# Performance work log

Hardware: AMD Instinct MI355X
Metric: run time of the kernel (lower is better)

Reference implementation:

```python
import jax, jax.numpy as jnp
import numpy as np

NUM_HEADS = 12
TOPK = 90


def setup_inputs() -> dict:
    key = jax.random.key(0)
    k1, k2, k3 = jax.random.split(key, 3)
    B, N, C = 8, 512, 768
    x = jax.random.normal(k1, (B, N, C), dtype=jnp.float32)
    qkv_w = jax.random.normal(k2, (3 * C, C), dtype=jnp.float32) * (C ** -0.5)
    proj_w = jax.random.normal(k3, (C, C), dtype=jnp.float32) * (C ** -0.5)
    proj_b = jnp.zeros((C,), dtype=jnp.float32)
    return {"x": x, "qkv_w": qkv_w, "proj_w": proj_w, "proj_b": proj_b, "islast": 0}


def reference(x, qkv_w, proj_w, proj_b, islast):
    B, N, C = x.shape
    H = NUM_HEADS
    hd = C // H
    scale = hd ** -0.5
    # qkv projection (no bias), split into q,k,v heads: [B,H,N,hd]
    qkv = (x @ qkv_w.T).reshape(B, N, 3, H, hd).transpose(2, 0, 3, 1, 4)
    q, k, v = qkv[0], qkv[1], qkv[2]
    attn = jnp.einsum('bhnd,bhmd->bhnm', q, k) * scale  # [B,H,N,N]
    if not islast:
        # keep only the top-k scores per row (kth-value threshold == topk mask)
        kth = jax.lax.top_k(attn, TOPK)[0][..., -1:]  # [B,H,N,1]
        attn = jnp.where(attn >= kth, attn, -jnp.inf)
    attn = jax.nn.softmax(attn, axis=-1)
    out = jnp.einsum('bhnm,bhmd->bnhd', attn, v).reshape(B, N, C)
    out = out @ proj_w.T + proj_b
    return out, attn
```

## Files before the change

### kernel.cpp

```cpp
#include <hip/hip_runtime.h>
#include <math.h>

#define BB 8
#define NN 512
#define CC 768
#define HH 12
#define HD 64
#define TOPK 90
#define QKV_ELEMS (BB*HH*NN*HD)
#define KC 2304

typedef __attribute__((ext_vector_type(8))) short short8;
typedef __attribute__((ext_vector_type(4))) float floatx4;

__device__ inline unsigned short f2bf(float f) {
    unsigned int u = __float_as_uint(f);
    u += 0x7FFFu + ((u >> 16) & 1u);
    return (unsigned short)(u >> 16);
}
__device__ inline float bf2f(unsigned short h) {
    return __uint_as_float(((unsigned int)h) << 16);
}

template<bool IS_A>
__global__ __launch_bounds__(256) void split_k(const float* __restrict__ in,
                                               unsigned short* __restrict__ o2,
                                               int total) {
    int idx = blockIdx.x * 256 + threadIdx.x;
    if (idx >= total) return;
    int e = idx * 4;
    int m = e / CC, kk = e - m * CC;
    float4 f = *(const float4*)(in + e);
    ushort4 hi, lo;
    hi.x = f2bf(f.x); lo.x = f2bf(f.x - bf2f(hi.x));
    hi.y = f2bf(f.y); lo.y = f2bf(f.y - bf2f(hi.y));
    hi.z = f2bf(f.z); lo.z = f2bf(f.z - bf2f(hi.z));
    hi.w = f2bf(f.w); lo.w = f2bf(f.w - bf2f(hi.w));
    unsigned short* base = o2 + (size_t)m * KC + kk;
    *(ushort4*)(base)        = hi;
    *(ushort4*)(base + CC)   = IS_A ? hi : lo;
    *(ushort4*)(base + 2*CC) = IS_A ? lo : hi;
}

template<int NCOLS, bool QKV_EPI>
__global__ __launch_bounds__(256) void gemm_split(const unsigned short* __restrict__ A,
                                                  const unsigned short* __restrict__ Bm,
                                                  const float* __restrict__ bias,
                                                  float* __restrict__ out,
                                                  unsigned short* __restrict__ qh,
                                                  unsigned short* __restrict__ ql,
                                                  unsigned short* __restrict__ kh,
                                                  unsigned short* __restrict__ kl,
                                                  float* __restrict__ vt) {
    __shared__ char lds[16384];
    const int bm = blockIdx.x, bn = blockIdx.y;
    const int tid  = threadIdx.x;
    const int wave = tid >> 6, lane = tid & 63;
    const int wm = wave >> 1, wn = wave & 1;
    const int quad = lane >> 4, r = lane & 15;

    const int cA0 = tid, cA1 = tid + 256;
    const int mA0 = cA0 >> 2, oA0 = (cA0 & 3) ^ ((mA0 >> 1) & 3);
    const int mA1 = cA1 >> 2, oA1 = (cA1 & 3) ^ ((mA1 >> 1) & 3);
    const unsigned short* gA0 = A  + (size_t)(bm*128 + mA0) * KC + oA0*8;
    const unsigned short* gA1 = A  + (size_t)(bm*128 + mA1) * KC + oA1*8;
    const unsigned short* gB0 = Bm + (size_t)(bn*128 + mA0) * KC + oA0*8;
    const unsigned short* gB1 = Bm + (size_t)(bn*128 + mA1) * KC + oA1*8;
    char* lA0 = lds + (wave*64)*16;
    char* lA1 = lds + (256 + wave*64)*16;
    char* lB0 = lds + 8192 + (wave*64)*16;
    char* lB1 = lds + 8192 + (256 + wave*64)*16;

    const int octsel = quad ^ ((r >> 1) & 3);
    int aoff[4], boff[4];
#pragma unroll
    for (int i = 0; i < 4; ++i) {
        aoff[i] = ((wm*64 + i*16 + r)*4 + octsel) * 16;
        boff[i] = 8192 + ((wn*64 + i*16 + r)*4 + octsel) * 16;
    }

    floatx4 acc[4][4];
#pragma unroll
    for (int i = 0; i < 4; ++i)
#pragma unroll
        for (int j = 0; j < 4; ++j)
            acc[i][j] = (floatx4){0.f, 0.f, 0.f, 0.f};

    for (int it = 0; it < KC/32; ++it) {
        __syncthreads();
        __builtin_amdgcn_global_load_lds((const __attribute__((address_space(1))) unsigned int*)gA0,
                                         (__attribute__((address_space(3))) unsigned int*)lA0, 16, 0, 0);
        __builtin_amdgcn_global_load_lds((const __attribute__((address_space(1))) unsigned int*)gA1,
                                         (__attribute__((address_space(3))) unsigned int*)lA1, 16, 0, 0);
        __builtin_amdgcn_global_load_lds((const __attribute__((address_space(1))) unsigned int*)gB0,
                                         (__attribute__((address_space(3))) unsigned int*)lB0, 16, 0, 0);
        __builtin_amdgcn_global_load_lds((const __attribute__((address_space(1))) unsigned int*)gB1,
                                         (__attribute__((address_space(3))) unsigned int*)lB1, 16, 0, 0);
        gA0 += 32; gA1 += 32; gB0 += 32; gB1 += 32;
        asm volatile("s_waitcnt vmcnt(0)" ::: "memory");
        __syncthreads();

        short8 af[4], bf[4];
#pragma unroll
        for (int i = 0; i < 4; ++i) af[i] = *(const short8*)(lds + aoff[i]);
#pragma unroll
        for (int j = 0; j < 4; ++j) bf[j] = *(const short8*)(lds + boff[j]);
#pragma unroll
        for (int i = 0; i < 4; ++i)
#pragma unroll
            for (int j = 0; j < 4; ++j)
                acc[i][j] = __builtin_amdgcn_mfma_f32_16x16x32_bf16(af[i], bf[j], acc[i][j], 0, 0, 0);
    }

    if (QKV_EPI) {
#pragma unroll
        for (int j = 0; j < 4; ++j) {
            int col = bn*128 + wn*64 + j*16 + r;
            int t = col / CC;
            int rem = col - t*CC;
            int h = rem >> 6, d = rem & 63;
            if (t == 2) {
#pragma unroll
                for (int i = 0; i < 4; ++i) {
                    int m0 = bm*128 + wm*64 + i*16 + quad*4;
                    int b = m0 >> 9, n0 = m0 & 511;
                    float4 o4 = {acc[i][j][0], acc[i][j][1], acc[i][j][2], acc[i][j][3]};
                    *(float4*)(vt + ((size_t)((b*HH + h)*HD + d))*NN + n0) = o4;
                }
            } else {
                unsigned short* ph = (t == 0) ? qh : kh;
                unsigned short* pl = (t == 0) ? ql : kl;
#pragma unroll
                for (int i = 0; i < 4; ++i) {
#pragma unroll
                    for (int e = 0; e < 4; ++e) {
                        int m = bm*128 + wm*64 + i*16 + quad*4 + e;
                        int b = m >> 9, nrow = m & 511;
                        size_t idx = ((size_t)(b*HH + h)*NN + nrow)*HD + d;
                        float val = acc[i][j][e];
                        unsigned short hi = f2bf(val);
                        ph[idx] = hi;
                        pl[idx] = f2bf(val - bf2f(hi));
                    }
                }
            }
        }
    } else {
#pragma unroll
        for (int j = 0; j < 4; ++j) {
            int col = bn*128 + wn*64 + j*16 + r;
            float bv = bias[col];
#pragma unroll
            for (int i = 0; i < 4; ++i) {
#pragma unroll
                for (int e = 0; e < 4; ++e) {
                    int m = bm*128 + wm*64 + i*16 + quad*4 + e;
                    out[(size_t)m*NCOLS + col] = acc[i][j][e] + bv;
                }
            }
        }
    }
}

__global__ __launch_bounds__(256, 1) void attn_scores_k(
        const unsigned short* __restrict__ qh, const unsigned short* __restrict__ ql,
        const unsigned short* __restrict__ kh, const unsigned short* __restrict__ kl,
        const int* __restrict__ islast, float* __restrict__ attn) {

    __shared__ unsigned short qs[2][64][72];
    __shared__ char ks[16384];

    const int bh = blockIdx.x % 96;
    const int rb = blockIdx.x / 96;
    const int tid = threadIdx.x;
    const int wv = tid >> 6, lane = tid & 63;
    const int quad = lane >> 4, r = lane & 15;

    const unsigned short* gq[2] = { qh + ((size_t)bh*NN + rb*64)*HD,
                                    ql + ((size_t)bh*NN + rb*64)*HD };
#pragma unroll
    for (int i = 0; i < 4; ++i) {
        int s = tid + i*256;
        int hl = s >> 9, s2 = s & 511;
        int row = s2 >> 3, oct = s2 & 7;
        short8 val = *(const short8*)(gq[hl] + row*HD + oct*8);
        *(short8*)&qs[hl][row][oct*8] = val;
    }
    __syncthreads();

    short8 afr[6];
    {
        const int arow = wv*16 + r;
#pragma unroll
        for (int t = 0; t < 3; ++t) {
            int src = (t == 2) ? 1 : 0;
#pragma unroll
            for (int half = 0; half < 2; ++half)
                afr[t*2+half] = *(const short8*)&qs[src][arow][half*32 + quad*8];
        }
    }

    floatx4 acc[32];
#pragma unroll
    for (int ct = 0; ct < 32; ++ct) acc[ct] = (floatx4){0.f,0.f,0.f,0.f};

    const unsigned short* gk[2] = { kh + (size_t)bh*NN*HD, kl + (size_t)bh*NN*HD };

    for (int ch = 0; ch < 8; ++ch) {
        __syncthreads();
#pragma unroll
        for (int i = 0; i < 4; ++i) {
            int s = tid + i*256;
            int hl = s >> 9, s2 = s & 511;
            int row = s2 >> 3, octp = s2 & 7;
            int oct = octp ^ (row & 7);
            const unsigned short* src = gk[hl] + (size_t)(ch*64 + row)*HD + oct*8;
            __builtin_amdgcn_global_load_lds(
                (const __attribute__((address_space(1))) unsigned int*)src,
                (__attribute__((address_space(3))) unsigned int*)(ks + (size_t)(i*256 + wv*64)*16),
                16, 0, 0);
        }
        asm volatile("s_waitcnt vmcnt(0)" ::: "memory");
        __syncthreads();

#pragma unroll
        for (int ctl = 0; ctl < 4; ++ctl) {
            const int ct = ch*4 + ctl;
            const int n = ctl*16 + r;
#pragma unroll
            for (int t = 0; t < 3; ++t) {
                const int srcB = (t == 1) ? 1 : 0;
#pragma unroll
                for (int half = 0; half < 2; ++half) {
                    const int oct = (half*4 + quad) ^ (n & 7);
                    short8 bfr = *(const short8*)(ks + srcB*8192 + n*128 + oct*16);
                    acc[ct] = __builtin_amdgcn_mfma_f32_16x16x32_bf16(afr[t*2+half], bfr, acc[ct], 0, 0, 0);
                }
            }
        }
    }

    const int lastv = islast[0];

#pragma unroll
    for (int e = 0; e < 4; ++e) {
        unsigned int key[32];
#pragma unroll
        for (int ct = 0; ct < 32; ++ct) {
            unsigned int t = __float_as_uint(acc[ct][e] * 0.125f);
            key[ct] = (t & 0x80000000u) ? ~t : (t | 0x80000000u);
        }

        unsigned int kth = 0u;
        if (!lastv) {
            unsigned int uo = key[0], ua = key[0];
#pragma unroll
            for (int ct = 1; ct < 32; ++ct) { uo |= key[ct]; ua &= key[ct]; }
#pragma unroll
            for (int off = 1; off <= 8; off <<= 1) {
                uo |= __shfl_xor(uo, off);
                ua &= __shfl_xor(ua, off);
            }
            unsigned int diff = uo ^ ua;
            int bit = 31 - __clz(diff);
            unsigned int am = 0xFFFFFFFFu;
            int kk = TOPK, cntA = 512;
            int done = (diff == 0u);
            while (__ballot(!done) != 0ull) {
                if (!done) {
                    unsigned int m1 = 0u;
#pragma unroll
                    for (int ct = 0; ct < 32; ++ct)
                        m1 |= ((key[ct] >> bit) & 1u) << ct;
                    int c1 = __popc(am & m1);
                    c1 += __shfl_xor(c1, 1);
                    c1 += __shfl_xor(c1, 2);
                    c1 += __shfl_xor(c1, 4);
                    c1 += __shfl_xor(c1, 8);
                    if (kk <= c1) { am &= m1; cntA = c1; }
                    else          { kk -= c1; am &= ~m1; cntA -= c1; }
                    --bit;
                    done = (cntA == kk) | (kk == 1) | (bit < 0);
                }
            }
            unsigned int mn = 0xFFFFFFFFu, mx = 0u;
#pragma unroll
            for (int ct = 0; ct < 32; ++ct) {
                if ((am >> ct) & 1u) {
                    mn = mn < key[ct] ? mn : key[ct];
                    mx = mx > key[ct] ? mx : key[ct];
                }
            }
#pragma unroll
            for (int off = 1; off <= 8; off <<= 1) {
                unsigned int mns = __shfl_xor(mn, off), mxs = __shfl_xor(mx, off);
                mn = mn < mns ? mn : mns; mx = mx > mxs ? mx : mxs;
            }
            kth = (kk == 1) ? mx : mn;
        }

        unsigned int umx = key[0];
#pragma unroll
        for (int ct = 1; ct < 32; ++ct) umx = umx > key[ct] ? umx : key[ct];
#pragma unroll
        for (int off = 1; off <= 8; off <<= 1) {
            unsigned int t2 = __shfl_xor(umx, off);
            umx = umx > t2 ? umx : t2;
        }
        float fmx = __uint_as_float((umx & 0x80000000u) ? (umx & 0x7FFFFFFFu) : ~umx);
        float sum = 0.f;
#pragma unroll
        for (int ct = 0; ct < 32; ++ct) {
            unsigned int uu = key[ct];
            float f = __uint_as_float((uu & 0x80000000u) ? (uu & 0x7FFFFFFFu) : ~uu);
            float ev = (lastv || uu >= kth) ? __expf(f - fmx) : 0.f;
            acc[ct][e] = ev;
            sum += ev;
        }
#pragma unroll
        for (int off = 1; off <= 8; off <<= 1) sum += __shfl_xor(sum, off);
        const float inv = 1.f / sum;
        float* arow = attn + ((size_t)bh*NN + rb*64 + wv*16 + quad*4 + e) * NN;
#pragma unroll
        for (int ct = 0; ct < 32; ++ct) arow[ct*16 + r] = acc[ct][e] * inv;
    }
}

__global__ __launch_bounds__(256) void attn_pv_k(const float* __restrict__ attn,
                                                 const float* __restrict__ vt,
                                                 unsigned short* __restrict__ Ao) {
    __shared__ unsigned short pls[64][72];
    __shared__ unsigned short vhs[64][72];
    __shared__ unsigned short vls[64][72];

    const int blk = blockIdx.x;
    const int bh  = blk % 96;
    const int rb  = blk / 96;
    const int b = bh / HH, h = bh % HH;
    const int tid = threadIdx.x;
    const int wv = tid >> 6, lane = tid & 63;
    const int quad = lane >> 4, r = lane & 15;

    const int sm = tid >> 2;
    const int sk = (tid & 3) * 16;
    const float* prow = attn + ((size_t)bh*NN + rb*64 + sm) * NN + sk;
    const float* vrow = vt + ((size_t)bh*HD + sm) * NN + sk;

    floatx4 accO[4];
#pragma unroll
    for (int j = 0; j < 4; ++j) accO[j] = (floatx4){0.f,0.f,0.f,0.f};

    for (int ch = 0; ch < 8; ++ch) {
        float pv[16], vv[16];
#pragma unroll
        for (int x = 0; x < 4; ++x) {
            *(float4*)&pv[x*4] = *(const float4*)(prow + ch*64 + x*4);
            *(float4*)&vv[x*4] = *(const float4*)(vrow + ch*64 + x*4);
        }
        __syncthreads();
        unsigned short tp[16], th[16], tl[16];
#pragma unroll
        for (int x = 0; x < 16; ++x) {
            tp[x] = f2bf(pv[x]);
            th[x] = f2bf(vv[x]);
            tl[x] = f2bf(vv[x] - bf2f(th[x]));
        }
        *(short8*)&pls[sm][sk]   = *(short8*)&tp[0];
        *(short8*)&pls[sm][sk+8] = *(short8*)&tp[8];
        *(short8*)&vhs[sm][sk]   = *(short8*)&th[0];
        *(short8*)&vhs[sm][sk+8] = *(short8*)&th[8];
        *(short8*)&vls[sm][sk]   = *(short8*)&tl[0];
        *(short8*)&vls[sm][sk+8] = *(short8*)&tl[8];
        __syncthreads();

#pragma unroll
        for (int kb = 0; kb < 2; ++kb) {
            short8 af = *(const short8*)&pls[wv*16 + r][kb*32 + quad*8];
#pragma unroll
            for (int j = 0; j < 4; ++j) {
                short8 bh8 = *(const short8*)&vhs[j*16 + r][kb*32 + quad*8];
                short8 bl8 = *(const short8*)&vls[j*16 + r][kb*32 + quad*8];
                accO[j] = __builtin_amdgcn_mfma_f32_16x16x32_bf16(af, bh8, accO[j], 0, 0, 0);
                accO[j] = __builtin_amdgcn_mfma_f32_16x16x32_bf16(af, bl8, accO[j], 0, 0, 0);
            }
        }
    }

#pragma unroll
    for (int j = 0; j < 4; ++j) {
        int d = j*16 + r;
#pragma unroll
        for (int e = 0; e < 4; ++e) {
            int n = rb*64 + wv*16 + quad*4 + e;
            size_t mrow = (size_t)b*NN + n;
            float val = accO[j][e];
            unsigned short hi = f2bf(val);
            unsigned short lo = f2bf(val - bf2f(hi));
            unsigned short* base = Ao + mrow*KC + h*HD + d;
            base[0] = hi; base[CC] = hi; base[2*CC] = lo;
        }
    }
}

extern "C" void kernel_launch(void* const* d_in, const int* in_sizes, int n_in,
                              void* d_out, int out_size, void* d_ws, size_t ws_size,
                              hipStream_t stream) {
    const float* x      = (const float*)d_in[0];
    const float* qkv_w  = (const float*)d_in[1];
    const float* proj_w = (const float*)d_in[2];
    const float* proj_b = (const float*)d_in[3];
    const int*   islast = (const int*)d_in[4];

    float* out  = (float*)d_out;
    float* attn = out + (size_t)BB*NN*CC;

    float* ws = (float*)d_ws;
    float* vt = ws;
    unsigned short* qhp = (unsigned short*)(ws + (size_t)QKV_ELEMS);
    unsigned short* qlp = qhp + (size_t)QKV_ELEMS;
    unsigned short* khp = qlp + (size_t)QKV_ELEMS;
    unsigned short* klp = khp + (size_t)QKV_ELEMS;
    unsigned short* Asp   = klp + (size_t)QKV_ELEMS;
    unsigned short* Bqkv  = Asp  + (size_t)4096*KC;
    unsigned short* Bproj = Bqkv + (size_t)2304*KC;

    split_k<true> <<<dim3(4096*CC/4/256), 256, 0, stream>>>(x,      Asp,   4096*CC/4);
    split_k<false><<<dim3(2304*CC/4/256), 256, 0, stream>>>(qkv_w,  Bqkv,  2304*CC/4);
    split_k<false><<<dim3(CC*CC/4/256),   256, 0, stream>>>(proj_w, Bproj, CC*CC/4);

    gemm_split<0, true>  <<<dim3(32, 18), 256, 0, stream>>>(Asp, Bqkv, nullptr, nullptr,
                                                            qhp, qlp, khp, klp, vt);
    attn_scores_k        <<<dim3(96*8),   256, 0, stream>>>(qhp, qlp, khp, klp, islast, attn);
    attn_pv_k            <<<dim3(96*8),   256, 0, stream>>>(attn, vt, Asp);
    gemm_split<CC, false><<<dim3(32, 6),  256, 0, stream>>>(Asp, Bproj, proj_b, out,
                                                            nullptr, nullptr, nullptr, nullptr, nullptr);
}
```

Baseline: 366.2 us.

## Fuse PV into scores kernel, pre-split V to bf16, deepen GEMM K-tile

Merges the attention-probability times V step into the scores kernel so the normalized probabilities stay in registers instead of being re-read from global memory. The QKV GEMM epilogue now writes V transposed as bf16 hi/lo pairs, so the fused kernel can stream V tiles straight into LDS with global_load_lds. The GEMM K-step grows from 32 to 64, using 32KB of LDS with an 8-way XOR swizzle, which halves the number of barrier and wait round-trips. The costs are higher LDS and register pressure in the fused kernel and one fewer launch-level stage of parallelism.

Result: faster. 356.3 us (-2.7%).

```diff
diff --git a/kernel.cpp b/kernel.cpp
--- a/kernel.cpp
+++ b/kernel.cpp
@@ -51,33 +51,35 @@
                                                   unsigned short* __restrict__ ql,
                                                   unsigned short* __restrict__ kh,
                                                   unsigned short* __restrict__ kl,
-                                                  float* __restrict__ vt) {
-    __shared__ char lds[16384];
+                                                  unsigned short* __restrict__ vth,
+                                                  unsigned short* __restrict__ vtl) {
+    __shared__ char lds[32768];
     const int bm = blockIdx.x, bn = blockIdx.y;
     const int tid  = threadIdx.x;
     const int wave = tid >> 6, lane = tid & 63;
     const int wm = wave >> 1, wn = wave & 1;
     const int quad = lane >> 4, r = lane & 15;
 
-    const int cA0 = tid, cA1 = tid + 256;
-    const int mA0 = cA0 >> 2, oA0 = (cA0 & 3) ^ ((mA0 >> 1) & 3);
-    const int mA1 = cA1 >> 2, oA1 = (cA1 & 3) ^ ((mA1 >> 1) & 3);
-    const unsigned short* gA0 = A  + (size_t)(bm*128 + mA0) * KC + oA0*8;
-    const unsigned short* gA1 = A  + (size_t)(bm*128 + mA1) * KC + oA1*8;
-    const unsigned short* gB0 = Bm + (size_t)(bn*128 + mA0) * KC + oA0*8;
-    const unsigned short* gB1 = Bm + (size_t)(bn*128 + mA1) * KC + oA1*8;
-    char* lA0 = lds + (wave*64)*16;
-    char* lA1 = lds + (256 + wave*64)*16;
-    char* lB0 = lds + 8192 + (wave*64)*16;
-    char* lB1 = lds + 8192 + (256 + wave*64)*16;
-
-    const int octsel = quad ^ ((r >> 1) & 3);
-    int aoff[4], boff[4];
-#pragma unroll
-    for (int i = 0; i < 4; ++i) {
-        aoff[i] = ((wm*64 + i*16 + r)*4 + octsel) * 16;
-        boff[i] = 8192 + ((wn*64 + i*16 + r)*4 + octsel) * 16;
-    }
+    const unsigned short* gbase[8];
+#pragma unroll
+    for (int i = 0; i < 8; ++i) {
+        int c = tid + i*256;
+        int s = c & 1023;
+        int m = s >> 3, octp = s & 7, oct = octp ^ (m & 7);
+        gbase[i] = (i < 4 ? A  + (size_t)(bm*128 + m) * KC
+                          : Bm + (size_t)(bn*128 + m) * KC) + oct*8;
+    }
+
+    int aoff[2][4], boff[2][4];
+#pragma unroll
+    for (int kb = 0; kb < 2; ++kb)
+#pragma unroll
+        for (int i = 0; i < 4; ++i) {
+            int ra = wm*64 + i*16 + r;
+            int rb2 = wn*64 + i*16 + r;
+            aoff[kb][i] = (ra*8 + ((kb*4 + quad) ^ (ra & 7))) * 16;
+            boff[kb][i] = 16384 + (rb2*8 + ((kb*4 + quad) ^ (rb2 & 7))) * 16;
+        }
 
     floatx4 acc[4][4];
 #pragma unroll
@@ -86,30 +88,32 @@
         for (int j = 0; j < 4; ++j)
             acc[i][j] = (floatx4){0.f, 0.f, 0.f, 0.f};
 
-    for (int it = 0; it < KC/32; ++it) {
-        __syncthreads();
-        __builtin_amdgcn_global_load_lds((const __attribute__((address_space(1))) unsigned int*)gA0,
-                                         (__attribute__((address_space(3))) unsigned int*)lA0, 16, 0, 0);
-        __builtin_amdgcn_global_load_lds((const __attribute__((address_space(1))) unsigned int*)gA1,
-                                         (__attribute__((address_space(3))) unsigned int*)lA1, 16, 0, 0);
-        __builtin_amdgcn_global_load_lds((const __attribute__((address_space(1))) unsigned int*)gB0,
-                                         (__attribute__((address_space(3))) unsigned int*)lB0, 16, 0, 0);
-        __builtin_amdgcn_global_load_lds((const __attribute__((address_space(1))) unsigned int*)gB1,
-                                         (__attribute__((address_space(3))) unsigned int*)lB1, 16, 0, 0);
-        gA0 += 32; gA1 += 32; gB0 += 32; gB1 += 32;
+    for (int it = 0; it < KC/64; ++it) {
+        __syncthreads();
+#pragma unroll
+        for (int i = 0; i < 8; ++i) {
+            __builtin_amdgcn_global_load_lds(
+                (const __attribute__((address_space(1))) unsigned int*)gbase[i],
+                (__attribute__((address_space(3))) unsigned int*)(lds + i*4096 + wave*1024),
+                16, 0, 0);
+            gbase[i] += 64;
+        }
         asm volatile("s_waitcnt vmcnt(0)" ::: "memory");
         __syncthreads();
 
-        short8 af[4], bf[4];
-#pragma unroll
-        for (int i = 0; i < 4; ++i) af[i] = *(const short8*)(lds + aoff[i]);
-#pragma unroll
-        for (int j = 0; j < 4; ++j) bf[j] = *(const short8*)(lds + boff[j]);
-#pragma unroll
-        for (int i = 0; i < 4; ++i)
-#pragma unroll
-            for (int j = 0; j < 4; ++j)
-                acc[i][j] = __builtin_amdgcn_mfma_f32_16x16x32_bf16(af[i], bf[j], acc[i][j], 0, 0, 0);
+#pragma unroll
+        for (int kb = 0; kb < 2; ++kb) {
+            short8 af[4], bf[4];
+#pragma unroll
+            for (int i = 0; i < 4; ++i) af[i] = *(const short8*)(lds + aoff[kb][i]);
+#pragma unroll
+            for (int j = 0; j < 4; ++j) bf[j] = *(const short8*)(lds + boff[kb][j]);
+#pragma unroll
+            for (int i = 0; i < 4; ++i)
+#pragma unroll
+                for (int j = 0; j < 4; ++j)
+                    acc[i][j] = __builtin_amdgcn_mfma_f32_16x16x32_bf16(af[i], bf[j], acc[i][j], 0, 0, 0);
+        }
     }
 
     if (QKV_EPI) {
@@ -124,8 +128,14 @@
                 for (int i = 0; i < 4; ++i) {
                     int m0 = bm*128 + wm*64 + i*16 + quad*4;
                     int b = m0 >> 9, n0 = m0 & 511;
-                    float4 o4 = {acc[i][j][0], acc[i][j][1], acc[i][j][2], acc[i][j][3]};
-                    *(float4*)(vt + ((size_t)((b*HH + h)*HD + d))*NN + n0) = o4;
+                    ushort4 hi, lo;
+                    hi.x = f2bf(acc[i][j][0]); lo.x = f2bf(acc[i][j][0] - bf2f(hi.x));
+                    hi.y = f2bf(acc[i][j][1]); lo.y = f2bf(acc[i][j][1] - bf2f(hi.y));
+                    hi.z = f2bf(acc[i][j][2]); lo.z = f2bf(acc[i][j][2] - bf2f(hi.z));
+                    hi.w = f2bf(acc[i][j][3]); lo.w = f2bf(acc[i][j][3] - bf2f(hi.w));
+                    size_t off = ((size_t)((b*HH + h)*HD + d))*NN + n0;
+                    *(ushort4*)(vth + off) = hi;
+                    *(ushort4*)(vtl + off) = lo;
                 }
             } else {
                 unsigned short* ph = (t == 0) ? qh : kh;
@@ -165,16 +175,20 @@
 __global__ __launch_bounds__(256, 1) void attn_scores_k(
         const unsigned short* __restrict__ qh, const unsigned short* __restrict__ ql,
         const unsigned short* __restrict__ kh, const unsigned short* __restrict__ kl,
-        const int* __restrict__ islast, float* __restrict__ attn) {
-
-    __shared__ unsigned short qs[2][64][72];
-    __shared__ char ks[16384];
+        const unsigned short* __restrict__ vth, const unsigned short* __restrict__ vtl,
+        const int* __restrict__ islast, float* __restrict__ attn,
+        unsigned short* __restrict__ Ao) {
+
+    __shared__ char smem[34816];
+    unsigned short* qs = (unsigned short*)smem;
+    char* ks = smem + 18432;
 
     const int bh = blockIdx.x % 96;
     const int rb = blockIdx.x / 96;
     const int tid = threadIdx.x;
     const int wv = tid >> 6, lane = tid & 63;
     const int quad = lane >> 4, r = lane & 15;
+    const int b = bh / HH, h = bh % HH;
 
     const unsigned short* gq[2] = { qh + ((size_t)bh*NN + rb*64)*HD,
                                     ql + ((size_t)bh*NN + rb*64)*HD };
@@ -184,7 +198,7 @@
         int hl = s >> 9, s2 = s & 511;
         int row = s2 >> 3, oct = s2 & 7;
         short8 val = *(const short8*)(gq[hl] + row*HD + oct*8);
-        *(short8*)&qs[hl][row][oct*8] = val;
+        *(short8*)&qs[(hl*64 + row)*72 + oct*8] = val;
     }
     __syncthreads();
 
@@ -196,7 +210,7 @@
             int src = (t == 2) ? 1 : 0;
 #pragma unroll
             for (int half = 0; half < 2; ++half)
-                afr[t*2+half] = *(const short8*)&qs[src][arow][half*32 + quad*8];
+                afr[t*2+half] = *(const short8*)&qs[(src*64 + arow)*72 + half*32 + quad*8];
         }
     }
 
@@ -322,64 +336,58 @@
         const float inv = 1.f / sum;
         float* arow = attn + ((size_t)bh*NN + rb*64 + wv*16 + quad*4 + e) * NN;
 #pragma unroll
-        for (int ct = 0; ct < 32; ++ct) arow[ct*16 + r] = acc[ct][e] * inv;
-    }
-}
-
-__global__ __launch_bounds__(256) void attn_pv_k(const float* __restrict__ attn,
-                                                 const float* __restrict__ vt,
-                                                 unsigned short* __restrict__ Ao) {
-    __shared__ unsigned short pls[64][72];
-    __shared__ unsigned short vhs[64][72];
-    __shared__ unsigned short vls[64][72];
-
-    const int blk = blockIdx.x;
-    const int bh  = blk % 96;
-    const int rb  = blk / 96;
-    const int b = bh / HH, h = bh % HH;
-    const int tid = threadIdx.x;
-    const int wv = tid >> 6, lane = tid & 63;
-    const int quad = lane >> 4, r = lane & 15;
-
-    const int sm = tid >> 2;
-    const int sk = (tid & 3) * 16;
-    const float* prow = attn + ((size_t)bh*NN + rb*64 + sm) * NN + sk;
-    const float* vrow = vt + ((size_t)bh*HD + sm) * NN + sk;
+        for (int ct = 0; ct < 32; ++ct) {
+            float p = acc[ct][e] * inv;
+            acc[ct][e] = p;
+            arow[ct*16 + r] = p;
+        }
+    }
+
+    unsigned short* pls = (unsigned short*)smem;
+    char* vhs = smem + 10240;
+    char* vls = smem + 18432;
+    const unsigned short* gvh = vth + (size_t)bh*HD*NN;
+    const unsigned short* gvl = vtl + (size_t)bh*HD*NN;
 
     floatx4 accO[4];
 #pragma unroll
     for (int j = 0; j < 4; ++j) accO[j] = (floatx4){0.f,0.f,0.f,0.f};
 
     for (int ch = 0; ch < 8; ++ch) {
-        float pv[16], vv[16];
-#pragma unroll
-        for (int x = 0; x < 4; ++x) {
-            *(float4*)&pv[x*4] = *(const float4*)(prow + ch*64 + x*4);
-            *(float4*)&vv[x*4] = *(const float4*)(vrow + ch*64 + x*4);
-        }
-        __syncthreads();
-        unsigned short tp[16], th[16], tl[16];
-#pragma unroll
-        for (int x = 0; x < 16; ++x) {
-            tp[x] = f2bf(pv[x]);
-            th[x] = f2bf(vv[x]);
-            tl[x] = f2bf(vv[x] - bf2f(th[x]));
-        }
-        *(short8*)&pls[sm][sk]   = *(short8*)&tp[0];
-        *(short8*)&pls[sm][sk+8] = *(short8*)&tp[8];
-        *(short8*)&vhs[sm][sk]   = *(short8*)&th[0];
-        *(short8*)&vhs[sm][sk+8] = *(short8*)&th[8];
-        *(short8*)&vls[sm][sk]   = *(short8*)&tl[0];
-        *(short8*)&vls[sm][sk+8] = *(short8*)&tl[8];
+        __syncthreads();
+#pragma unroll
+        for (int ctl = 0; ctl < 4; ++ctl) {
+            int col = ctl*16 + r;
+#pragma unroll
+            for (int e = 0; e < 4; ++e)
+                pls[(wv*16 + quad*4 + e)*80 + col] = f2bf(acc[ch*4 + ctl][e]);
+        }
+#pragma unroll
+        for (int i = 0; i < 2; ++i) {
+            int s = tid + i*256;
+            int d = s >> 3, octp = s & 7, oct = octp ^ (d & 7);
+            size_t goff = (size_t)d*NN + ch*64 + oct*8;
+            __builtin_amdgcn_global_load_lds(
+                (const __attribute__((address_space(1))) unsigned int*)(gvh + goff),
+                (__attribute__((address_space(3))) unsigned int*)(vhs + (i*256 + wv*64)*16),
+                16, 0, 0);
+            __builtin_amdgcn_global_load_lds(
+                (const __attribute__((address_space(1))) unsigned int*)(gvl + goff),
+                (__attribute__((address_space(3))) unsigned int*)(vls + (i*256 + wv*64)*16),
+                16, 0, 0);
+        }
+        asm volatile("s_waitcnt vmcnt(0)" ::: "memory");
         __syncthreads();
 
 #pragma unroll
         for (int kb = 0; kb < 2; ++kb) {
-            short8 af = *(const short8*)&pls[wv*16 + r][kb*32 + quad*8];
+            short8 af = *(const short8*)&pls[(wv*16 + r)*80 + kb*32 + quad*8];
 #pragma unroll
             for (int j = 0; j < 4; ++j) {
-                short8 bh8 = *(const short8*)&vhs[j*16 + r][kb*32 + quad*8];
-                short8 bl8 = *(const short8*)&vls[j*16 + r][kb*32 + quad*8];
+                int d = j*16 + r;
+                int oct = (kb*4 + quad) ^ (d & 7);
+                short8 bh8 = *(const short8*)(vhs + d*128 + oct*16);
+                short8 bl8 = *(const short8*)(vls + d*128 + oct*16);
                 accO[j] = __builtin_amdgcn_mfma_f32_16x16x32_bf16(af, bh8, accO[j], 0, 0, 0);
                 accO[j] = __builtin_amdgcn_mfma_f32_16x16x32_bf16(af, bl8, accO[j], 0, 0, 0);
             }
@@ -414,9 +422,10 @@
     float* out  = (float*)d_out;
     float* attn = out + (size_t)BB*NN*CC;
 
-    float* ws = (float*)d_ws;
-    float* vt = ws;
-    unsigned short* qhp = (unsigned short*)(ws + (size_t)QKV_ELEMS);
+    unsigned short* us = (unsigned short*)d_ws;
+    unsigned short* vth = us;
+    unsigned short* vtl = vth + (size_t)QKV_ELEMS;
+    unsigned short* qhp = vtl + (size_t)QKV_ELEMS;
     unsigned short* qlp = qhp + (size_t)QKV_ELEMS;
     unsigned short* khp = qlp + (size_t)QKV_ELEMS;
     unsigned short* klp = khp + (size_t)QKV_ELEMS;
@@ -429,9 +438,10 @@
     split_k<false><<<dim3(CC*CC/4/256),   256, 0, stream>>>(proj_w, Bproj, CC*CC/4);
 
     gemm_split<0, true>  <<<dim3(32, 18), 256, 0, stream>>>(Asp, Bqkv, nullptr, nullptr,
-                                                            qhp, qlp, khp, klp, vt);
-    attn_scores_k        <<<dim3(96*8),   256, 0, stream>>>(qhp, qlp, khp, klp, islast, attn);
-    attn_pv_k            <<<dim3(96*8),   256, 0, stream>>>(attn, vt, Asp);
+                                                            qhp, qlp, khp, klp, vth, vtl);
+    attn_scores_k        <<<dim3(96*8),   256, 0, stream>>>(qhp, qlp, khp, klp, vth, vtl,
+                                                            islast, attn, Asp);
     gemm_split<CC, false><<<dim3(32, 6),  256, 0, stream>>>(Asp, Bproj, proj_b, out,
-                                                            nullptr, nullptr, nullptr, nullptr, nullptr);
-}
+                                                            nullptr, nullptr, nullptr, nullptr,
+                                                            nullptr, nullptr);
+}
```
